# Kernel tuning notes

Measured on AMD Instinct MI355X. Metric: run time of the kernel, lower is better.

The kernel has to match this reference:

```python
import jax, jax.numpy as jnp
import numpy as np

T, B, E = 2048, 2, 1024
H = 16
D = E // H


def setup_inputs() -> dict:
    key = jax.random.key(0)
    ks = jax.random.split(key, 7)
    s = 1.0 / np.sqrt(E)
    return {
        "query": jax.random.normal(ks[0], (T, B, E), jnp.float32),
        "key": jax.random.normal(ks[1], (T, B, E), jnp.float32),
        "value": jax.random.normal(ks[2], (T, B, E), jnp.float32),
        "in_proj_weight": jax.random.normal(ks[3], (3 * E, E), jnp.float32) * s,
        "in_proj_bias": jax.random.normal(ks[4], (3 * E,), jnp.float32) * 0.02,
        "out_proj_weight": jax.random.normal(ks[5], (E, E), jnp.float32) * s,
        "out_proj_bias": jax.random.normal(ks[6], (E,), jnp.float32) * 0.02,
    }


def reference(query, key, value, in_proj_weight, in_proj_bias, out_proj_weight, out_proj_bias):
    tgt_len, bsz, embed_dim = query.shape
    src_len = key.shape[0]
    head_dim = embed_dim // H
    # packed in-projection (F.linear: x @ W.T + b)
    w_q, w_k, w_v = jnp.split(in_proj_weight, 3, axis=0)
    b_q, b_k, b_v = jnp.split(in_proj_bias, 3, axis=0)
    q = query @ w_q.T + b_q   # [T, B, E]
    k = key @ w_k.T + b_k     # [S, B, E]
    v = value @ w_v.T + b_v   # [S, B, E]
    # [T,B,E] -> [B,H,T,D]
    q = q.reshape(tgt_len, bsz, H, head_dim).transpose(1, 2, 0, 3)
    k = k.reshape(src_len, bsz, H, head_dim).transpose(1, 2, 0, 3)
    v = v.reshape(src_len, bsz, H, head_dim).transpose(1, 2, 0, 3)
    scale = 1.0 / jnp.sqrt(jnp.asarray(head_dim, q.dtype))
    scores = jnp.einsum("bhtd,bhsd->bhts", q, k) * scale  # [B,H,T,S]
    attn_weights = jax.nn.softmax(scores, axis=-1)
    attn = jnp.einsum("bhts,bhsd->bhtd", attn_weights, v)  # [B,H,T,D]
    # [B,H,T,D] -> [T,B,E]
    attn = attn.transpose(2, 0, 1, 3).reshape(tgt_len, bsz, embed_dim)
    attn_output = attn @ out_proj_weight.T + out_proj_bias  # [T,B,E]
    # averaged attention weights over heads (average_attn_weights=True)
    avg_weights = jnp.sum(attn_weights, axis=1) / H  # [B,T,S]
    return attn_output, avg_weights
```

## Files before the change

### kernel.cpp

```cpp
#include <hip/hip_runtime.h>
#include <hip/hip_bf16.h>

typedef float  f32x2  __attribute__((ext_vector_type(2)));
typedef float  f32x4  __attribute__((ext_vector_type(4)));
typedef float  f32x16 __attribute__((ext_vector_type(16)));
typedef __bf16 bf16x8 __attribute__((ext_vector_type(8)));

#define MFMA16(A,B,C) __builtin_amdgcn_mfma_f32_16x16x32_bf16((A),(B),(C),0,0,0)
#define MFMA32(A,B,C) __builtin_amdgcn_mfma_f32_32x32x16_bf16((A),(B),(C),0,0,0)
#define EXP2(x) __builtin_amdgcn_exp2f(x)
#define LOG2(x) __builtin_amdgcn_logf(x)

static constexpr int Tn = 2048, Bn = 2, En = 1024, Hn = 16, Dn = 64;
static constexpr float kQScale = 0.125f * 1.4426950408889634f;

static __device__ __forceinline__ unsigned pack2(float a, float b) {
  union { __bf16 h[2]; unsigned u; } un;
  un.h[0] = (__bf16)a; un.h[1] = (__bf16)b;
  return un.u;
}

static __device__ __forceinline__ void gload_lds16(const void* g, void* l) {
  __builtin_amdgcn_global_load_lds(
      (const __attribute__((address_space(1))) void*)g,
      (__attribute__((address_space(3))) void*)l, 16, 0, 0);
}

__global__ __launch_bounds__(256)
void k_cvt(const float* __restrict__ q, const float* __restrict__ k,
           const float* __restrict__ v, const float* __restrict__ w3,
           const float* __restrict__ wo,
           __bf16* __restrict__ qb, __bf16* __restrict__ kb,
           __bf16* __restrict__ vb, __bf16* __restrict__ w3b,
           __bf16* __restrict__ wob)
{
  const size_t g = (size_t)blockIdx.x * 256 + threadIdx.x;
  const float* src;
  __bf16* dst;
  size_t off;
  if (g < 524288)        { src = q;  dst = qb;  off = g; }
  else if (g < 1048576)  { src = k;  dst = kb;  off = g - 524288; }
  else if (g < 1572864)  { src = v;  dst = vb;  off = g - 1048576; }
  else if (g < 1966080)  { src = w3; dst = w3b; off = g - 1572864; }
  else                   { src = wo; dst = wob; off = g - 1966080; }
  const float* p = src + off * 8;
  f32x4 a = *reinterpret_cast<const f32x4*>(p);
  f32x4 b = *reinterpret_cast<const f32x4*>(p + 4);
  bf16x8 o;
  #pragma unroll
  for (int e = 0; e < 4; ++e) { o[e] = (__bf16)a[e]; o[e + 4] = (__bf16)b[e]; }
  *reinterpret_cast<bf16x8*>(dst + off * 8) = o;
}

__global__ __launch_bounds__(256)
void k_qkv(const __bf16* __restrict__ Xq, const __bf16* __restrict__ Xk,
           const __bf16* __restrict__ Xv, const __bf16* __restrict__ W,
           const float* __restrict__ bias,
           __bf16* __restrict__ q_ws, __bf16* __restrict__ k_ws,
           __bf16* __restrict__ v_ws)
{
  __shared__ __align__(16) char a_lds[2][8192];
  __shared__ __align__(16) char b_lds[2][8192];
  const int tid = threadIdx.x;
  const int lane = tid & 63, w = tid >> 6;
  const int wr = w >> 1, wc = w & 1;
  const int ag = lane >> 4, lr = lane & 15;
  const int mBase = blockIdx.x * 128;
  const int oBase = blockIdx.y * 128;
  const int which = blockIdx.y >> 3;
  const __bf16* X  = (which == 0) ? Xq : ((which == 1) ? Xk : Xv);
  const __bf16* Wt = W + (size_t)oBase * En;
  __bf16* dst = (which == 0) ? q_ws : ((which == 1) ? k_ws : v_ws);
  const float oscale = (which == 0) ? kQScale : 1.0f;

  const int gA = w;
  const __bf16* pa0 = X  + (size_t)(mBase + lane) * En + gA * 8;
  const __bf16* pa1 = X  + (size_t)(mBase + 64 + lane) * En + gA * 8;
  const __bf16* pb0 = Wt + (size_t)(lane) * En + gA * 8;
  const __bf16* pb1 = Wt + (size_t)(64 + lane) * En + gA * 8;

  f32x4 acc[4][4];
  #pragma unroll
  for (int i = 0; i < 4; ++i)
    #pragma unroll
    for (int j = 0; j < 4; ++j) { f32x4 z = {0.f, 0.f, 0.f, 0.f}; acc[i][j] = z; }

  gload_lds16(pa0, &a_lds[0][gA * 2048]);
  gload_lds16(pa1, &a_lds[0][gA * 2048 + 1024]);
  gload_lds16(pb0, &b_lds[0][gA * 2048]);
  gload_lds16(pb1, &b_lds[0][gA * 2048 + 1024]);
  __syncthreads();

  for (int kt = 0; kt < 32; ++kt) {
    const int cur = kt & 1, nxt = cur ^ 1;
    if (kt + 1 < 32) {
      const int kk = (kt + 1) * 32;
      gload_lds16(pa0 + kk, &a_lds[nxt][gA * 2048]);
      gload_lds16(pa1 + kk, &a_lds[nxt][gA * 2048 + 1024]);
      gload_lds16(pb0 + kk, &b_lds[nxt][gA * 2048]);
      gload_lds16(pb1 + kk, &b_lds[nxt][gA * 2048 + 1024]);
    }
    bf16x8 af[4], bfr[4];
    #pragma unroll
    for (int mb = 0; mb < 4; ++mb)
      af[mb] = *(const bf16x8*)(&a_lds[cur][ag * 2048 + (wr * 64 + mb * 16 + lr) * 16]);
    #pragma unroll
    for (int nb = 0; nb < 4; ++nb)
      bfr[nb] = *(const bf16x8*)(&b_lds[cur][ag * 2048 + (wc * 64 + nb * 16 + lr) * 16]);
    #pragma unroll
    for (int mb = 0; mb < 4; ++mb)
      #pragma unroll
      for (int nb = 0; nb < 4; ++nb)
        acc[mb][nb] = MFMA16(af[mb], bfr[nb], acc[mb][nb]);
    __syncthreads();
  }

  #pragma unroll
  for (int nb = 0; nb < 4; ++nb) {
    int oG = oBase + wc * 64 + nb * 16 + lr;
    float bv = bias[oG];
    int oS = oG & (En - 1);
    int h = oS >> 6, d = oS & 63;
    #pragma unroll
    for (int mb = 0; mb < 4; ++mb)
      #pragma unroll
      for (int r = 0; r < 4; ++r) {
        int i = mBase + wr * 64 + mb * 16 + ag * 4 + r;
        int t = i >> 1, b2 = i & 1;
        dst[(((size_t)(b2 * Hn + h)) * Tn + t) * Dn + d] =
            (__bf16)((acc[mb][nb][r] + bv) * oscale);
      }
  }
}

__global__ __launch_bounds__(256)
void k_transpose_v(const __bf16* __restrict__ v_ws, __bf16* __restrict__ vt_ws)
{
  __shared__ __bf16 tile[64][72];
  const int bh = blockIdx.x >> 5;
  const int tt = blockIdx.x & 31;
  const int tid = threadIdx.x;
  const __bf16* src = v_ws + ((size_t)bh * Tn + tt * 64) * Dn;
  #pragma unroll
  for (int it = 0; it < 2; ++it) {
    int gi = tid + it * 256;
    int row = gi >> 3, gg = gi & 7;
    *reinterpret_cast<bf16x8*>(&tile[row][gg * 8]) =
        *reinterpret_cast<const bf16x8*>(src + row * Dn + gg * 8);
  }
  __syncthreads();
  __bf16* dst = vt_ws + (size_t)bh * Dn * Tn + tt * 64;
  #pragma unroll
  for (int it = 0; it < 2; ++it) {
    int gi = tid + it * 256;
    int drow = gi >> 3, tg = gi & 7;
    bf16x8 vv;
    #pragma unroll
    for (int e = 0; e < 8; ++e) vv[e] = tile[tg * 8 + e][drow];
    *reinterpret_cast<bf16x8*>(dst + (size_t)drow * Tn + tg * 8) = vv;
  }
}

__global__ __launch_bounds__(256, 2)
void k_flash(const __bf16* __restrict__ q_ws, const __bf16* __restrict__ k_ws,
             const __bf16* __restrict__ vt_ws, __bf16* __restrict__ ctx,
             float* __restrict__ adj_g)
{
  __shared__ __align__(16) char kv_sm[2 * 16384];

  const int tid = threadIdx.x;
  const int lane = tid & 63, w = tid >> 6;
  const int tl = lane & 31, hi = lane >> 5;
  const int bh = blockIdx.x >> 4;
  const int qt = blockIdx.x & 15;
  const int t0w = qt * 128 + w * 32;

  const __bf16* kbase  = k_ws + (size_t)bh * Tn * Dn;
  const __bf16* vtbase = vt_ws + (size_t)bh * Dn * Tn;

  bf16x8 qf[4];
  {
    const __bf16* qrow = q_ws + ((size_t)bh * Tn + t0w + tl) * Dn + hi * 8;
    #pragma unroll
    for (int c = 0; c < 4; ++c)
      qf[c] = *reinterpret_cast<const bf16x8*>(qrow + c * 16);
  }

  union { unsigned u[4]; bf16x8 v; } onu;
  #pragma unroll
  for (int j = 0; j < 4; ++j) onu.u[j] = 0x3F803F80u;
  const bf16x8 kOne = onu.v;

  f32x16 accO0, accO1, accL;
  #pragma unroll
  for (int i = 0; i < 16; ++i) { accO0[i] = 0.f; accO1[i] = 0.f; accL[i] = 0.f; }
  float m_run = -INFINITY;

  const int r0 = tid >> 3, s0 = tid & 7;
  const int ldso = ((s0 ^ (r0 & 7)) << 4);
  const int ko0 = r0 * 128 + ldso;

  bf16x8 rk0 = *(const bf16x8*)(kbase + r0 * 64 + s0 * 8);
  bf16x8 rk1 = *(const bf16x8*)(kbase + (r0 + 32) * 64 + s0 * 8);
  bf16x8 rv0 = *(const bf16x8*)(vtbase + (size_t)r0 * Tn + s0 * 8);
  bf16x8 rv1 = *(const bf16x8*)(vtbase + (size_t)(r0 + 32) * Tn + s0 * 8);
  *(bf16x8*)(kv_sm + ko0) = rk0;
  *(bf16x8*)(kv_sm + ko0 + 4096) = rk1;
  *(bf16x8*)(kv_sm + 8192 + ko0) = rv0;
  *(bf16x8*)(kv_sm + 8192 + ko0 + 4096) = rv1;

  for (int st = 0; st < 32; ++st) {
    __syncthreads();
    const char* cur = kv_sm + (st & 1) * 16384;
    char* nxt = kv_sm + ((st + 1) & 1) * 16384;
    if (st + 1 < 32) {
      const __bf16* kn = kbase + (size_t)(st + 1) * 64 * Dn;
      const __bf16* vn = vtbase + (st + 1) * 64;
      rk0 = *(const bf16x8*)(kn + r0 * 64 + s0 * 8);
      rk1 = *(const bf16x8*)(kn + (r0 + 32) * 64 + s0 * 8);
      rv0 = *(const bf16x8*)(vn + (size_t)r0 * Tn + s0 * 8);
      rv1 = *(const bf16x8*)(vn + (size_t)(r0 + 32) * Tn + s0 * 8);
    }

    f32x16 sc0, sc1;
    #pragma unroll
    for (int i = 0; i < 16; ++i) { sc0[i] = 0.f; sc1[i] = 0.f; }
    const char* kr0 = cur + tl * 128;
    const char* kr1 = cur + (32 + tl) * 128;
    __builtin_amdgcn_s_setprio(1);
    #pragma unroll
    for (int c = 0; c < 4; ++c) {
      const int off = (((2 * c + hi) ^ (tl & 7)) << 4);
      sc0 = MFMA32(*(const bf16x8*)(kr0 + off), qf[c], sc0);
      sc1 = MFMA32(*(const bf16x8*)(kr1 + off), qf[c], sc1);
    }
    __builtin_amdgcn_s_setprio(0);

    float mx[8];
    #pragma unroll
    for (int i = 0; i < 8; ++i)
      mx[i] = fmaxf(fmaxf(sc0[i], sc0[i + 8]), fmaxf(sc1[i], sc1[i + 8]));
    float tm = fmaxf(fmaxf(fmaxf(mx[0], mx[1]), fmaxf(mx[2], mx[3])),
                     fmaxf(fmaxf(mx[4], mx[5]), fmaxf(mx[6], mx[7])));
    tm = fmaxf(tm, __shfl_xor(tm, 32, 64));
    if (__any(tm > m_run + 8.0f)) {
      const float mn = fmaxf(m_run, tm);
      const float es = EXP2(m_run - mn);
      m_run = mn;
      #pragma unroll
      for (int q = 0; q < 4; ++q)
        #pragma unroll
        for (int rr = 0; rr < 4; ++rr) {
          const float e = __shfl(es, 8 * q + 4 * hi + rr, 32);
          accO0[q * 4 + rr] *= e;
          accO1[q * 4 + rr] *= e;
          accL[q * 4 + rr] *= e;
        }
    }
    #pragma unroll
    for (int i = 0; i < 16; ++i) {
      sc0[i] = EXP2(sc0[i] - m_run);
      sc1[i] = EXP2(sc1[i] - m_run);
    }

    unsigned wA0[4], wB0[4], wA1[4], wB1[4];
    #pragma unroll
    for (int g = 0; g < 4; ++g) {
      wA0[g] = pack2(sc0[4 * g],     sc0[4 * g + 1]);
      wB0[g] = pack2(sc0[4 * g + 2], sc0[4 * g + 3]);
      wA1[g] = pack2(sc1[4 * g],     sc1[4 * g + 1]);
      wB1[g] = pack2(sc1[4 * g + 2], sc1[4 * g + 3]);
    }
    bf16x8 pa[2][2];
    #pragma unroll
    for (int sb = 0; sb < 2; ++sb) {
      const unsigned* WA = sb ? wA1 : wA0;
      const unsigned* WB = sb ? wB1 : wB0;
      #pragma unroll
      for (int c = 0; c < 2; ++c) {
        unsigned w0 = WA[2 * c], w2 = WA[2 * c + 1];
        unsigned w1 = WB[2 * c], w3 = WB[2 * c + 1];
        asm("v_permlane32_swap_b32 %0, %1" : "+v"(w0), "+v"(w2));
        asm("v_permlane32_swap_b32 %0, %1" : "+v"(w1), "+v"(w3));
        union { unsigned u[4]; bf16x8 v; } uu;
        uu.u[0] = w0; uu.u[1] = w1; uu.u[2] = w2; uu.u[3] = w3;
        pa[sb][c] = uu.v;
      }
    }

    const char* vr0 = cur + 8192 + tl * 128;
    const char* vr1 = cur + 8192 + (32 + tl) * 128;
    __builtin_amdgcn_s_setprio(1);
    #pragma unroll
    for (int sb = 0; sb < 2; ++sb)
      #pragma unroll
      for (int c = 0; c < 2; ++c) {
        const int off = (((sb * 4 + c * 2 + hi) ^ (tl & 7)) << 4);
        accO0 = MFMA32(pa[sb][c], *(const bf16x8*)(vr0 + off), accO0);
        accO1 = MFMA32(pa[sb][c], *(const bf16x8*)(vr1 + off), accO1);
        accL  = MFMA32(pa[sb][c], kOne, accL);
      }
    __builtin_amdgcn_s_setprio(0);

    if (st + 1 < 32) {
      *(bf16x8*)(nxt + ko0) = rk0;
      *(bf16x8*)(nxt + ko0 + 4096) = rk1;
      *(bf16x8*)(nxt + 8192 + ko0) = rv0;
      *(bf16x8*)(nxt + 8192 + ko0 + 4096) = rv1;
    }
  }

  const int b2 = bh >> 4, h = bh & 15;
  float adjv[16];
  #pragma unroll
  for (int q = 0; q < 4; ++q)
    #pragma unroll
    for (int rr = 0; rr < 4; ++rr) {
      const int j = q * 4 + rr;
      const float lv = 1.0f / accL[j];
      const int t = t0w + 8 * q + 4 * hi + rr;
      __bf16* cp = ctx + ((size_t)t * Bn + b2) * En + h * 64 + tl;
      cp[0]  = (__bf16)(accO0[j] * lv);
      cp[32] = (__bf16)(accO1[j] * lv);
      const float mrow = __shfl(m_run, 8 * q + 4 * hi + rr, 32);
      adjv[j] = mrow + LOG2(16.0f * accL[j]);
    }
  if (tl == 0) {
    #pragma unroll
    for (int q = 0; q < 4; ++q)
      #pragma unroll
      for (int rr = 0; rr < 4; ++rr) {
        const int t = t0w + 8 * q + 4 * hi + rr;
        adj_g[(size_t)bh * Tn + t] = adjv[q * 4 + rr];
      }
  }
}

__global__ __launch_bounds__(256)
void k_avgw(const __bf16* __restrict__ q_ws, const __bf16* __restrict__ k_ws,
            const float* __restrict__ adj_g, float* __restrict__ avg_out)
{
  __shared__ __align__(16) char q_sm[2][8192];
  __shared__ __align__(16) char k_sm[2][8192];
  __shared__ __align__(16) float adj_sm[16][64];

  const int tid = threadIdx.x;
  const int lane = tid & 63, w = tid >> 6;
  const int tl = lane & 31, hi = lane >> 5;
  const int b2 = blockIdx.x >> 10;
  const int tt = (blockIdx.x >> 5) & 31;
  const int ss = blockIdx.x & 31;
  const int thalf = (w >> 1) * 32, shalf = (w & 1) * 32;

  #pragma unroll
  for (int it = 0; it < 4; ++it) {
    int idx = tid + it * 256;
    int h = idx >> 6, trow = idx & 63;
    adj_sm[h][trow] = adj_g[((size_t)(b2 * Hn + h)) * Tn + tt * 64 + trow];
  }

  const size_t hstride = (size_t)Tn * Dn;
  const __bf16* qb = q_ws + ((size_t)(b2 * Hn) * Tn + tt * 64) * Dn;
  const __bf16* kb = k_ws + ((size_t)(b2 * Hn) * Tn + ss * 64) * Dn;

  const int r0 = tid >> 3, s0 = tid & 7;
  const int ldso = ((s0 ^ (r0 & 7)) << 4);
  const int ko0 = r0 * 128 + ldso;

  bf16x8 rq0 = *(const bf16x8*)(qb + r0 * 64 + s0 * 8);
  bf16x8 rq1 = *(const bf16x8*)(qb + (r0 + 32) * 64 + s0 * 8);
  bf16x8 rk0 = *(const bf16x8*)(kb + r0 * 64 + s0 * 8);
  bf16x8 rk1 = *(const bf16x8*)(kb + (r0 + 32) * 64 + s0 * 8);
  *(bf16x8*)(q_sm[0] + ko0) = rq0;
  *(bf16x8*)(q_sm[0] + ko0 + 4096) = rq1;
  *(bf16x8*)(k_sm[0] + ko0) = rk0;
  *(bf16x8*)(k_sm[0] + ko0 + 4096) = rk1;

  f32x16 avg;
  #pragma unroll
  for (int i = 0; i < 16; ++i) avg[i] = 0.f;

  for (int h = 0; h < Hn; ++h) {
    __syncthreads();
    const char* qc = q_sm[h & 1];
    const char* kc = k_sm[h & 1];
    char* qn = q_sm[(h + 1) & 1];
    char* kn = k_sm[(h + 1) & 1];
    if (h + 1 < Hn) {
      const __bf16* qp = qb + (size_t)(h + 1) * hstride;
      const __bf16* kp = kb + (size_t)(h + 1) * hstride;
      rq0 = *(const bf16x8*)(qp + r0 * 64 + s0 * 8);
      rq1 = *(const bf16x8*)(qp + (r0 + 32) * 64 + s0 * 8);
      rk0 = *(const bf16x8*)(kp + r0 * 64 + s0 * 8);
      rk1 = *(const bf16x8*)(kp + (r0 + 32) * 64 + s0 * 8);
    }

    f32x16 sc;
    #pragma unroll
    for (int i = 0; i < 16; ++i) sc[i] = 0.f;
    const char* qr = qc + (thalf + tl) * 128;
    const char* kr = kc + (shalf + tl) * 128;
    #pragma unroll
    for (int c = 0; c < 4; ++c) {
      const int off = (((2 * c + hi) ^ (tl & 7)) << 4);
      sc = MFMA32(*(const bf16x8*)(qr + off), *(const bf16x8*)(kr + off), sc);
    }

    #pragma unroll
    for (int q = 0; q < 4; ++q) {
      f32x4 ad = *(const f32x4*)&adj_sm[h][thalf + 8 * q + 4 * hi];
      #pragma unroll
      for (int r = 0; r < 4; ++r)
        avg[q * 4 + r] += EXP2(sc[q * 4 + r] - ad[r]);
    }

    if (h + 1 < Hn) {
      *(bf16x8*)(qn + ko0) = rq0;
      *(bf16x8*)(qn + ko0 + 4096) = rq1;
      *(bf16x8*)(kn + ko0) = rk0;
      *(bf16x8*)(kn + ko0 + 4096) = rk1;
    }
  }

  #pragma unroll
  for (int q = 0; q < 4; ++q)
    #pragma unroll
    for (int r = 0; r < 4; ++r) {
      int t = tt * 64 + thalf + 8 * q + 4 * hi + r;
      int s = ss * 64 + shalf + tl;
      avg_out[((size_t)(b2 * Tn + t)) * Tn + s] = avg[q * 4 + r];
    }
}

__global__ __launch_bounds__(256)
void k_outproj(const __bf16* __restrict__ ctx, const __bf16* __restrict__ W,
               const float* __restrict__ bias, float* __restrict__ out)
{
  __shared__ __align__(16) char a_lds[2][8192];
  __shared__ __align__(16) char b_lds[2][8192];
  const int tid = threadIdx.x;
  const int lane = tid & 63, w = tid >> 6;
  const int wr = w >> 1, wc = w & 1;
  const int ag = lane >> 4, lr = lane & 15;
  const int mBase = blockIdx.x * 128;
  const int oBase = blockIdx.y * 128;
  const __bf16* Wt = W + (size_t)oBase * En;

  const int gA = w;
  const __bf16* pa0 = ctx + (size_t)(mBase + lane) * En + gA * 8;
  const __bf16* pa1 = ctx + (size_t)(mBase + 64 + lane) * En + gA * 8;
  const __bf16* pb0 = Wt + (size_t)(lane) * En + gA * 8;
  const __bf16* pb1 = Wt + (size_t)(64 + lane) * En + gA * 8;

  f32x4 acc[4][4];
  #pragma unroll
  for (int i = 0; i < 4; ++i)
    #pragma unroll
    for (int j = 0; j < 4; ++j) { f32x4 z = {0.f,0.f,0.f,0.f}; acc[i][j] = z; }

  gload_lds16(pa0, &a_lds[0][gA * 2048]);
  gload_lds16(pa1, &a_lds[0][gA * 2048 + 1024]);
  gload_lds16(pb0, &b_lds[0][gA * 2048]);
  gload_lds16(pb1, &b_lds[0][gA * 2048 + 1024]);
  __syncthreads();

  for (int kt = 0; kt < 32; ++kt) {
    const int cur = kt & 1, nxt = cur ^ 1;
    if (kt + 1 < 32) {
      const int kk = (kt + 1) * 32;
      gload_lds16(pa0 + kk, &a_lds[nxt][gA * 2048]);
      gload_lds16(pa1 + kk, &a_lds[nxt][gA * 2048 + 1024]);
      gload_lds16(pb0 + kk, &b_lds[nxt][gA * 2048]);
      gload_lds16(pb1 + kk, &b_lds[nxt][gA * 2048 + 1024]);
    }
    bf16x8 af[4], bfr[4];
    #pragma unroll
    for (int mb = 0; mb < 4; ++mb)
      af[mb] = *(const bf16x8*)(&a_lds[cur][ag * 2048 + (wr * 64 + mb * 16 + lr) * 16]);
    #pragma unroll
    for (int nb = 0; nb < 4; ++nb)
      bfr[nb] = *(const bf16x8*)(&b_lds[cur][ag * 2048 + (wc * 64 + nb * 16 + lr) * 16]);
    #pragma unroll
    for (int mb = 0; mb < 4; ++mb)
      #pragma unroll
      for (int nb = 0; nb < 4; ++nb)
        acc[mb][nb] = MFMA16(af[mb], bfr[nb], acc[mb][nb]);
    __syncthreads();
  }

  #pragma unroll
  for (int nb = 0; nb < 4; ++nb) {
    int o = oBase + wc * 64 + nb * 16 + lr;
    float bv = bias[o];
    #pragma unroll
    for (int mb = 0; mb < 4; ++mb)
      #pragma unroll
      for (int r = 0; r < 4; ++r) {
        int i = mBase + wr * 64 + mb * 16 + ag * 4 + r;
        out[(size_t)i * En + o] = acc[mb][nb][r] + bv;
      }
  }
}

extern "C" void kernel_launch(void* const* d_in, const int* in_sizes, int n_in,
                              void* d_out, int out_size, void* d_ws, size_t ws_size,
                              hipStream_t stream)
{
  (void)in_sizes; (void)n_in; (void)out_size; (void)ws_size;
  const float* query = (const float*)d_in[0];
  const float* key   = (const float*)d_in[1];
  const float* value = (const float*)d_in[2];
  const float* in_w  = (const float*)d_in[3];
  const float* in_b  = (const float*)d_in[4];
  const float* out_w = (const float*)d_in[5];
  const float* out_b = (const float*)d_in[6];

  float* attn_out = (float*)d_out;
  float* avg_out  = (float*)d_out + (size_t)Tn * Bn * En;

  char* ws = (char*)d_ws;
  const size_t MB = 1u << 20;
  __bf16* q_ws  = (__bf16*)(ws);
  __bf16* k_ws  = (__bf16*)(ws + 8 * MB);
  __bf16* v_ws  = (__bf16*)(ws + 16 * MB);
  __bf16* vt_ws = (__bf16*)(ws + 24 * MB);
  __bf16* ctx   = (__bf16*)(ws + 32 * MB);
  float*  adj_g = (float*)(ws + 40 * MB);
  __bf16* xq_bf = vt_ws;
  __bf16* xk_bf = ctx;
  __bf16* xv_bf = (__bf16*)(ws + 40 * MB + 512 * 1024);
  __bf16* w3_bf = (__bf16*)(ws + 48 * MB + 512 * 1024);
  __bf16* wo_bf = (__bf16*)(ws + 54 * MB + 512 * 1024);

  k_cvt<<<8192, 256, 0, stream>>>(query, key, value, in_w, out_w,
                                  xq_bf, xk_bf, xv_bf, w3_bf, wo_bf);
  k_qkv<<<dim3(32, 24), 256, 0, stream>>>(xq_bf, xk_bf, xv_bf, w3_bf, in_b,
                                          q_ws, k_ws, v_ws);
  k_transpose_v<<<1024, 256, 0, stream>>>(v_ws, vt_ws);
  k_flash<<<512, 256, 0, stream>>>(q_ws, k_ws, vt_ws, ctx, adj_g);
  k_avgw<<<2048, 256, 0, stream>>>(q_ws, k_ws, adj_g, avg_out);
  k_outproj<<<dim3(32, 8), 256, 0, stream>>>(ctx, wo_bf, out_b, attn_out);
}
```

Measured before the change: 201.2 us.

## Triple-buffer QKV GEMM loads and halve out-proj tile width for more blocks

The QKV projection GEMM moves from double to triple-buffered LDS staging with explicit vmcnt waits and raw barriers, so global-to-LDS loads run two k-steps ahead of the MFMA work. The out-projection kernel switches to 128x64 tiles and doubles its grid to 512 blocks, which fills more compute units on a 256-block problem. The QKV loop issues a wrapped dummy stage in its last two iterations, and the smaller out-proj tiles reload the activation matrix twice as often.

```diff
diff --git a/kernel.cpp b/kernel.cpp
--- a/kernel.cpp
+++ b/kernel.cpp
@@ -59,8 +59,8 @@
            __bf16* __restrict__ q_ws, __bf16* __restrict__ k_ws,
            __bf16* __restrict__ v_ws)
 {
-  __shared__ __align__(16) char a_lds[2][8192];
-  __shared__ __align__(16) char b_lds[2][8192];
+  __shared__ __align__(16) char a_lds[3][8192];
+  __shared__ __align__(16) char b_lds[3][8192];
   const int tid = threadIdx.x;
   const int lane = tid & 63, w = tid >> 6;
   const int wr = w >> 1, wc = w & 1;
@@ -79,41 +79,48 @@
   const __bf16* pb0 = Wt + (size_t)(lane) * En + gA * 8;
   const __bf16* pb1 = Wt + (size_t)(64 + lane) * En + gA * 8;
 
+#define STAGE(J, KK) do {                                                    \
+    char* ab = a_lds[(J)];                                                   \
+    char* bb = b_lds[(J)];                                                   \
+    gload_lds16(pa0 + (KK), ab + gA * 2048);                                 \
+    gload_lds16(pa1 + (KK), ab + gA * 2048 + 1024);                         \
+    gload_lds16(pb0 + (KK), bb + gA * 2048);                                 \
+    gload_lds16(pb1 + (KK), bb + gA * 2048 + 1024);                         \
+  } while (0)
+
   f32x4 acc[4][4];
   #pragma unroll
   for (int i = 0; i < 4; ++i)
     #pragma unroll
     for (int j = 0; j < 4; ++j) { f32x4 z = {0.f, 0.f, 0.f, 0.f}; acc[i][j] = z; }
 
-  gload_lds16(pa0, &a_lds[0][gA * 2048]);
-  gload_lds16(pa1, &a_lds[0][gA * 2048 + 1024]);
-  gload_lds16(pb0, &b_lds[0][gA * 2048]);
-  gload_lds16(pb1, &b_lds[0][gA * 2048 + 1024]);
-  __syncthreads();
+  STAGE(0, 0);
+  STAGE(1, 32);
 
   for (int kt = 0; kt < 32; ++kt) {
-    const int cur = kt & 1, nxt = cur ^ 1;
-    if (kt + 1 < 32) {
-      const int kk = (kt + 1) * 32;
-      gload_lds16(pa0 + kk, &a_lds[nxt][gA * 2048]);
-      gload_lds16(pa1 + kk, &a_lds[nxt][gA * 2048 + 1024]);
-      gload_lds16(pb0 + kk, &b_lds[nxt][gA * 2048]);
-      gload_lds16(pb1 + kk, &b_lds[nxt][gA * 2048 + 1024]);
-    }
+    STAGE((kt + 2) % 3, ((kt + 2) & 31) * 32);
+    asm volatile("s_waitcnt vmcnt(8)" ::: "memory");
+    __builtin_amdgcn_s_barrier();
+    __builtin_amdgcn_sched_barrier(0);
+    const char* ac = a_lds[kt % 3];
+    const char* bc = b_lds[kt % 3];
     bf16x8 af[4], bfr[4];
     #pragma unroll
     for (int mb = 0; mb < 4; ++mb)
-      af[mb] = *(const bf16x8*)(&a_lds[cur][ag * 2048 + (wr * 64 + mb * 16 + lr) * 16]);
+      af[mb] = *(const bf16x8*)(ac + ag * 2048 + (wr * 64 + mb * 16 + lr) * 16);
     #pragma unroll
     for (int nb = 0; nb < 4; ++nb)
-      bfr[nb] = *(const bf16x8*)(&b_lds[cur][ag * 2048 + (wc * 64 + nb * 16 + lr) * 16]);
+      bfr[nb] = *(const bf16x8*)(bc + ag * 2048 + (wc * 64 + nb * 16 + lr) * 16);
     #pragma unroll
     for (int mb = 0; mb < 4; ++mb)
       #pragma unroll
       for (int nb = 0; nb < 4; ++nb)
         acc[mb][nb] = MFMA16(af[mb], bfr[nb], acc[mb][nb]);
-    __syncthreads();
-  }
+    asm volatile("s_waitcnt lgkmcnt(0)" ::: "memory");
+    __builtin_amdgcn_sched_barrier(0);
+    __builtin_amdgcn_s_barrier();
+  }
+#undef STAGE
 
   #pragma unroll
   for (int nb = 0; nb < 4; ++nb) {
@@ -388,11 +395,11 @@
     char* kn = k_sm[(h + 1) & 1];
     if (h + 1 < Hn) {
       const __bf16* qp = qb + (size_t)(h + 1) * hstride;
-      const __bf16* kp = kb + (size_t)(h + 1) * hstride;
+      const __bf16* kp2 = kb + (size_t)(h + 1) * hstride;
       rq0 = *(const bf16x8*)(qp + r0 * 64 + s0 * 8);
       rq1 = *(const bf16x8*)(qp + (r0 + 32) * 64 + s0 * 8);
-      rk0 = *(const bf16x8*)(kp + r0 * 64 + s0 * 8);
-      rk1 = *(const bf16x8*)(kp + (r0 + 32) * 64 + s0 * 8);
+      rk0 = *(const bf16x8*)(kp2 + r0 * 64 + s0 * 8);
+      rk1 = *(const bf16x8*)(kp2 + (r0 + 32) * 64 + s0 * 8);
     }
 
     f32x16 sc;
@@ -437,51 +444,54 @@
                const float* __restrict__ bias, float* __restrict__ out)
 {
   __shared__ __align__(16) char a_lds[2][8192];
-  __shared__ __align__(16) char b_lds[2][8192];
+  __shared__ __align__(16) char b_lds[2][4096];
   const int tid = threadIdx.x;
   const int lane = tid & 63, w = tid >> 6;
-  const int wr = w >> 1, wc = w & 1;
   const int ag = lane >> 4, lr = lane & 15;
   const int mBase = blockIdx.x * 128;
-  const int oBase = blockIdx.y * 128;
-  const __bf16* Wt = W + (size_t)oBase * En;
-
-  const int gA = w;
-  const __bf16* pa0 = ctx + (size_t)(mBase + lane) * En + gA * 8;
-  const __bf16* pa1 = ctx + (size_t)(mBase + 64 + lane) * En + gA * 8;
-  const __bf16* pb0 = Wt + (size_t)(lane) * En + gA * 8;
-  const __bf16* pb1 = Wt + (size_t)(64 + lane) * En + gA * 8;
-
-  f32x4 acc[4][4];
-  #pragma unroll
-  for (int i = 0; i < 4; ++i)
+  const int oBase = blockIdx.y * 64;
+
+  const int srow = (w & 1) * 64 + lane;
+  const int gw = w >> 1;
+  const __bf16* paj[2];
+  int aD[2];
+  #pragma unroll
+  for (int j = 0; j < 2; ++j) {
+    const int g = 2 * j + gw;
+    paj[j] = ctx + (size_t)(mBase + srow) * En + g * 8;
+    aD[j] = g * 2048 + (w & 1) * 1024;
+  }
+  const __bf16* pb = W + (size_t)(oBase + lane) * En + w * 8;
+  const int bDst = w * 1024;
+
+  f32x4 acc[2][4];
+  #pragma unroll
+  for (int i = 0; i < 2; ++i)
     #pragma unroll
     for (int j = 0; j < 4; ++j) { f32x4 z = {0.f,0.f,0.f,0.f}; acc[i][j] = z; }
 
-  gload_lds16(pa0, &a_lds[0][gA * 2048]);
-  gload_lds16(pa1, &a_lds[0][gA * 2048 + 1024]);
-  gload_lds16(pb0, &b_lds[0][gA * 2048]);
-  gload_lds16(pb1, &b_lds[0][gA * 2048 + 1024]);
+  #pragma unroll
+  for (int j = 0; j < 2; ++j) gload_lds16(paj[j], &a_lds[0][aD[j]]);
+  gload_lds16(pb, &b_lds[0][bDst]);
   __syncthreads();
 
   for (int kt = 0; kt < 32; ++kt) {
     const int cur = kt & 1, nxt = cur ^ 1;
     if (kt + 1 < 32) {
       const int kk = (kt + 1) * 32;
-      gload_lds16(pa0 + kk, &a_lds[nxt][gA * 2048]);
-      gload_lds16(pa1 + kk, &a_lds[nxt][gA * 2048 + 1024]);
-      gload_lds16(pb0 + kk, &b_lds[nxt][gA * 2048]);
-      gload_lds16(pb1 + kk, &b_lds[nxt][gA * 2048 + 1024]);
-    }
-    bf16x8 af[4], bfr[4];
-    #pragma unroll
-    for (int mb = 0; mb < 4; ++mb)
-      af[mb] = *(const bf16x8*)(&a_lds[cur][ag * 2048 + (wr * 64 + mb * 16 + lr) * 16]);
+      #pragma unroll
+      for (int j = 0; j < 2; ++j) gload_lds16(paj[j] + kk, &a_lds[nxt][aD[j]]);
+      gload_lds16(pb + kk, &b_lds[nxt][bDst]);
+    }
+    bf16x8 af[2], bfr[4];
+    #pragma unroll
+    for (int mb = 0; mb < 2; ++mb)
+      af[mb] = *(const bf16x8*)(&a_lds[cur][ag * 2048 + (w * 32 + mb * 16 + lr) * 16]);
     #pragma unroll
     for (int nb = 0; nb < 4; ++nb)
-      bfr[nb] = *(const bf16x8*)(&b_lds[cur][ag * 2048 + (wc * 64 + nb * 16 + lr) * 16]);
-    #pragma unroll
-    for (int mb = 0; mb < 4; ++mb)
+      bfr[nb] = *(const bf16x8*)(&b_lds[cur][ag * 1024 + (nb * 16 + lr) * 16]);
+    #pragma unroll
+    for (int mb = 0; mb < 2; ++mb)
       #pragma unroll
       for (int nb = 0; nb < 4; ++nb)
         acc[mb][nb] = MFMA16(af[mb], bfr[nb], acc[mb][nb]);
@@ -490,13 +500,13 @@
 
   #pragma unroll
   for (int nb = 0; nb < 4; ++nb) {
-    int o = oBase + wc * 64 + nb * 16 + lr;
+    int o = oBase + nb * 16 + lr;
     float bv = bias[o];
     #pragma unroll
-    for (int mb = 0; mb < 4; ++mb)
+    for (int mb = 0; mb < 2; ++mb)
       #pragma unroll
       for (int r = 0; r < 4; ++r) {
-        int i = mBase + wr * 64 + mb * 16 + ag * 4 + r;
+        int i = mBase + w * 32 + mb * 16 + ag * 4 + r;
         out[(size_t)i * En + o] = acc[mb][nb][r] + bv;
       }
   }
@@ -539,5 +549,5 @@
   k_transpose_v<<<1024, 256, 0, stream>>>(v_ws, vt_ws);
   k_flash<<<512, 256, 0, stream>>>(q_ws, k_ws, vt_ws, ctx, adj_g);
   k_avgw<<<2048, 256, 0, stream>>>(q_ws, k_ws, adj_g, avg_out);
-  k_outproj<<<dim3(32, 8), 256, 0, stream>>>(ctx, wo_bf, out_b, attn_out);
-}
+  k_outproj<<<dim3(32, 16), 256, 0, stream>>>(ctx, wo_bf, out_b, attn_out);
+}
```

Result: slower. 212.1 us (+5.4%).

## Split flash attention over key halves and merge partials in a combine kernel

Applied to the files above, without the earlier changes.

The flash kernel now processes only half of the key/value sequence per block, doubling the grid from 512 to 1024 blocks. It writes unnormalized partial outputs and per-row max and sum to workspace. A new combine kernel merges the two halves with log-sum-exp weights and produces ctx and the log-normalizer used by the averaging kernel. This targets low occupancy on a GPU with many compute units, at the cost of an extra launch, extra global traffic, and bf16 rounding of the unnormalized partials.

```diff
diff --git a/kernel.cpp b/kernel.cpp
--- a/kernel.cpp
+++ b/kernel.cpp
@@ -163,20 +163,23 @@
 
 __global__ __launch_bounds__(256, 2)
 void k_flash(const __bf16* __restrict__ q_ws, const __bf16* __restrict__ k_ws,
-             const __bf16* __restrict__ vt_ws, __bf16* __restrict__ ctx,
-             float* __restrict__ adj_g)
+             const __bf16* __restrict__ vt_ws,
+             __bf16* __restrict__ po0, __bf16* __restrict__ po1,
+             float* __restrict__ pml)
 {
   __shared__ __align__(16) char kv_sm[2 * 16384];
 
   const int tid = threadIdx.x;
   const int lane = tid & 63, w = tid >> 6;
   const int tl = lane & 31, hi = lane >> 5;
-  const int bh = blockIdx.x >> 4;
-  const int qt = blockIdx.x & 15;
+  const int bid = blockIdx.x;
+  const int bh = bid >> 5;
+  const int qt = (bid >> 1) & 15;
+  const int sh = bid & 1;
   const int t0w = qt * 128 + w * 32;
 
-  const __bf16* kbase  = k_ws + (size_t)bh * Tn * Dn;
-  const __bf16* vtbase = vt_ws + (size_t)bh * Dn * Tn;
+  const __bf16* kbase  = k_ws + (size_t)bh * Tn * Dn + (size_t)sh * 1024 * Dn;
+  const __bf16* vtbase = vt_ws + (size_t)bh * Dn * Tn + sh * 1024;
 
   bf16x8 qf[4];
   {
@@ -209,11 +212,11 @@
   *(bf16x8*)(kv_sm + 8192 + ko0) = rv0;
   *(bf16x8*)(kv_sm + 8192 + ko0 + 4096) = rv1;
 
-  for (int st = 0; st < 32; ++st) {
+  for (int st = 0; st < 16; ++st) {
     __syncthreads();
     const char* cur = kv_sm + (st & 1) * 16384;
     char* nxt = kv_sm + ((st + 1) & 1) * 16384;
-    if (st + 1 < 32) {
+    if (st + 1 < 16) {
       const __bf16* kn = kbase + (size_t)(st + 1) * 64 * Dn;
       const __bf16* vn = vtbase + (st + 1) * 64;
       rk0 = *(const bf16x8*)(kn + r0 * 64 + s0 * 8);
@@ -302,7 +305,7 @@
       }
     __builtin_amdgcn_s_setprio(0);
 
-    if (st + 1 < 32) {
+    if (st + 1 < 16) {
       *(bf16x8*)(nxt + ko0) = rk0;
       *(bf16x8*)(nxt + ko0 + 4096) = rk1;
       *(bf16x8*)(nxt + 8192 + ko0) = rv0;
@@ -310,30 +313,65 @@
     }
   }
 
-  const int b2 = bh >> 4, h = bh & 15;
-  float adjv[16];
+  __bf16* pob = (sh ? po1 : po0) + (size_t)bh * Tn * 64;
+  float mv[16], lv[16];
   #pragma unroll
   for (int q = 0; q < 4; ++q)
     #pragma unroll
     for (int rr = 0; rr < 4; ++rr) {
       const int j = q * 4 + rr;
-      const float lv = 1.0f / accL[j];
-      const int t = t0w + 8 * q + 4 * hi + rr;
-      __bf16* cp = ctx + ((size_t)t * Bn + b2) * En + h * 64 + tl;
-      cp[0]  = (__bf16)(accO0[j] * lv);
-      cp[32] = (__bf16)(accO1[j] * lv);
-      const float mrow = __shfl(m_run, 8 * q + 4 * hi + rr, 32);
-      adjv[j] = mrow + LOG2(16.0f * accL[j]);
+      const int tp = 8 * q + 4 * hi + rr;
+      const int t = t0w + tp;
+      __bf16* op = pob + (size_t)t * 64 + tl;
+      op[0]  = (__bf16)accO0[j];
+      op[32] = (__bf16)accO1[j];
+      mv[j] = __shfl(m_run, tp, 32);
+      lv[j] = accL[j];
     }
   if (tl == 0) {
+    float* pm = pml + ((size_t)(sh * 32 + bh) * Tn) * 2;
     #pragma unroll
     for (int q = 0; q < 4; ++q)
       #pragma unroll
       for (int rr = 0; rr < 4; ++rr) {
+        const int j = q * 4 + rr;
         const int t = t0w + 8 * q + 4 * hi + rr;
-        adj_g[(size_t)bh * Tn + t] = adjv[q * 4 + rr];
+        f32x2 s; s[0] = mv[j]; s[1] = lv[j];
+        *reinterpret_cast<f32x2*>(&pm[(size_t)t * 2]) = s;
       }
   }
+}
+
+__global__ __launch_bounds__(256)
+void k_comb(const __bf16* __restrict__ po0, const __bf16* __restrict__ po1,
+            const float* __restrict__ pml,
+            __bf16* __restrict__ ctx, float* __restrict__ adj_g)
+{
+  const int tid = threadIdx.x;
+  const int bh = blockIdx.x >> 6;
+  const int tc = blockIdx.x & 63;
+  const int trow = tid >> 3, g = tid & 7;
+  const int t = tc * 32 + trow;
+  const size_t i0 = (size_t)bh * Tn + t;
+
+  f32x2 s0 = *(const f32x2*)&pml[i0 * 2];
+  f32x2 s1 = *(const f32x2*)&pml[((size_t)(32 + bh) * Tn + t) * 2];
+  const float m = fmaxf(s0[0], s1[0]);
+  const float e0 = EXP2(s0[0] - m), e1 = EXP2(s1[0] - m);
+  const float l = s0[1] * e0 + s1[1] * e1;
+  const float w0 = e0 / l, w1 = e1 / l;
+
+  bf16x8 o0 = *(const bf16x8*)(po0 + i0 * 64 + g * 8);
+  bf16x8 o1 = *(const bf16x8*)(po1 + i0 * 64 + g * 8);
+  bf16x8 o;
+  #pragma unroll
+  for (int e = 0; e < 8; ++e)
+    o[e] = (__bf16)((float)o0[e] * w0 + (float)o1[e] * w1);
+
+  const int b2 = bh >> 4, h = bh & 15;
+  *reinterpret_cast<bf16x8*>(ctx + ((size_t)t * Bn + b2) * En + h * 64 + g * 8) = o;
+  if (g == 0)
+    adj_g[i0] = m + LOG2(16.0f * l);
 }
 
 __global__ __launch_bounds__(256)
@@ -388,11 +426,11 @@
     char* kn = k_sm[(h + 1) & 1];
     if (h + 1 < Hn) {
       const __bf16* qp = qb + (size_t)(h + 1) * hstride;
-      const __bf16* kp = kb + (size_t)(h + 1) * hstride;
+      const __bf16* kp2 = kb + (size_t)(h + 1) * hstride;
       rq0 = *(const bf16x8*)(qp + r0 * 64 + s0 * 8);
       rq1 = *(const bf16x8*)(qp + (r0 + 32) * 64 + s0 * 8);
-      rk0 = *(const bf16x8*)(kp + r0 * 64 + s0 * 8);
-      rk1 = *(const bf16x8*)(kp + (r0 + 32) * 64 + s0 * 8);
+      rk0 = *(const bf16x8*)(kp2 + r0 * 64 + s0 * 8);
+      rk1 = *(const bf16x8*)(kp2 + (r0 + 32) * 64 + s0 * 8);
     }
 
     f32x16 sc;
@@ -531,13 +569,17 @@
   __bf16* xv_bf = (__bf16*)(ws + 40 * MB + 512 * 1024);
   __bf16* w3_bf = (__bf16*)(ws + 48 * MB + 512 * 1024);
   __bf16* wo_bf = (__bf16*)(ws + 54 * MB + 512 * 1024);
+  __bf16* po0   = v_ws;
+  __bf16* po1   = xv_bf;
+  float*  pml   = (float*)(ws + 56 * MB + 512 * 1024);
 
   k_cvt<<<8192, 256, 0, stream>>>(query, key, value, in_w, out_w,
                                   xq_bf, xk_bf, xv_bf, w3_bf, wo_bf);
   k_qkv<<<dim3(32, 24), 256, 0, stream>>>(xq_bf, xk_bf, xv_bf, w3_bf, in_b,
                                           q_ws, k_ws, v_ws);
   k_transpose_v<<<1024, 256, 0, stream>>>(v_ws, vt_ws);
-  k_flash<<<512, 256, 0, stream>>>(q_ws, k_ws, vt_ws, ctx, adj_g);
+  k_flash<<<1024, 256, 0, stream>>>(q_ws, k_ws, vt_ws, po0, po1, pml);
+  k_comb<<<2048, 256, 0, stream>>>(po0, po1, pml, ctx, adj_g);
   k_avgw<<<2048, 256, 0, stream>>>(q_ws, k_ws, adj_g, avg_out);
   k_outproj<<<dim3(32, 8), 256, 0, stream>>>(ctx, wo_bf, out_b, attn_out);
 }
```

Result: slower. 206.1 us (+2.4%).
